# Optimization experiments

Measured on AMD Instinct MI355X. Metric: run time of the kernel, lower is better.

Reference implementation:

```python
import jax, jax.numpy as jnp
import numpy as np

N = 100000
E = 1600000
IN_FEATS = 512
N_CLASSES = 40
H1, D1 = 8, 8
H2, D2 = 1, N_CLASSES


def gat_conv(x, src, dst, W, al, ar, b, H, D):
    # x: [N, F] -> h: [N, H, D]
    n = x.shape[0]
    h = (x @ W).reshape(n, H, D)
    el = (h * al[None]).sum(-1)  # [N, H]
    er = (h * ar[None]).sum(-1)  # [N, H]
    e = jax.nn.leaky_relu(el[src] + er[dst], 0.2)  # [E, H]
    # segment softmax over destination neighborhoods
    emax = jax.ops.segment_max(e, dst, num_segments=n)  # [N, H]
    ee = jnp.exp(e - emax[dst])
    denom = jax.ops.segment_sum(ee, dst, num_segments=n)  # [N, H]
    a = ee / (denom[dst] + 1e-9)  # [E, H]
    m = h[src] * a[:, :, None]  # [E, H, D]
    out = jax.ops.segment_sum(m, dst, num_segments=n)  # [N, H, D]
    return out + b.reshape(1, H, D)


def setup_inputs() -> dict:
    key = jax.random.key(0)
    ks = jax.random.split(key, 12)
    g1 = 1.0 / np.sqrt(IN_FEATS)
    g2 = 1.0 / np.sqrt(H1 * D1)
    return {
        "x": jax.random.normal(ks[0], (N, IN_FEATS), jnp.float32),
        "src": jax.random.randint(ks[1], (E,), 0, N, jnp.int32),
        "dst": jax.random.randint(ks[2], (E,), 0, N, jnp.int32),
        "W1": jax.random.normal(ks[3], (IN_FEATS, H1 * D1), jnp.float32) * g1,
        "al1": jax.random.normal(ks[4], (H1, D1), jnp.float32) * 0.1,
        "ar1": jax.random.normal(ks[5], (H1, D1), jnp.float32) * 0.1,
        "b1": jnp.zeros((H1 * D1,), jnp.float32),
        "W2": jax.random.normal(ks[6], (H1 * D1, H2 * D2), jnp.float32) * g2,
        "al2": jax.random.normal(ks[7], (H2, D2), jnp.float32) * 0.1,
        "ar2": jax.random.normal(ks[8], (H2, D2), jnp.float32) * 0.1,
        "b2": jnp.zeros((H2 * D2,), jnp.float32),
    }


def reference(x, src, dst, W1, al1, ar1, b1, W2, al2, ar2, b2):
    h = gat_conv(x, src, dst, W1, al1, ar1, b1, H1, D1)  # [N, 8, 8]
    h = jax.nn.elu(h.reshape(N, H1 * D1))  # [N, 64]
    h = gat_conv(h, src, dst, W2, al2, ar2, b2, H2, D2).mean(axis=1)  # [N, n_classes]
    return jax.nn.log_softmax(h, axis=1)
```

## Files before the change

### kernel.cpp

```cpp
#include <hip/hip_runtime.h>
#include <hip/hip_bf16.h>
#include <math.h>

#define NCLS 40
#define PWG 256
#define BSH 9
#define NBMAX 512
#define SRCB 23
#define CSRCAP 14336

typedef __attribute__((ext_vector_type(8))) short bf16x8;
typedef __attribute__((ext_vector_type(4))) float f32x4;

__device__ inline float bf2f(ushort u) {
    unsigned v = ((unsigned)u) << 16;
    float f;
    __builtin_memcpy(&f, &v, 4);
    return f;
}
__device__ inline ushort f2bf(float f) {
    unsigned v;
    __builtin_memcpy(&v, &f, 4);
    unsigned r = (v + 0x7FFFu + ((v >> 16) & 1u)) >> 16;
    return (ushort)r;
}

__global__ __launch_bounds__(256) void conv_prep_kernel(
    const float* __restrict__ W1, ushort* __restrict__ W1t,
    const float* __restrict__ W2, const float* __restrict__ al2,
    const float* __restrict__ ar2, float* __restrict__ wal2,
    float* __restrict__ war2)
{
    if (blockIdx.x < 128) {
        int id = blockIdx.x * 256 + threadIdx.x;
        int k = id >> 6, c = id & 63;
        W1t[c * 512 + k] = f2bf(W1[k * 64 + c]);
    } else {
        int k = threadIdx.x;
        if (k < 64) {
            float a = 0.f, b = 0.f;
            for (int c = 0; c < NCLS; c++) {
                float w = W2[k * NCLS + c];
                a += w * al2[c];
                b += w * ar2[c];
            }
            wal2[k] = a;
            war2[k] = b;
        }
    }
}

__global__ __launch_bounds__(256) void gemm1_mfma_kernel(
    const float* __restrict__ x, const ushort* __restrict__ W1t,
    ushort* __restrict__ h1b, int Nn)
{
    __shared__ ushort As[64 * 40];
    __shared__ ushort Bs[64 * 40];
    const int t = threadIdx.x;
    const int lane = t & 63, w = t >> 6;
    const int tile = blockIdx.x * 64;

    f32x4 acc[4] = {};

    const int sr = t >> 2;
    const int sk = (t & 3) * 8;
    const int arow = tile + sr;
    const bool rowok = arow < Nn;
    const float* xrow = x + (size_t)arow * 512;
    const ushort* wrow = W1t + (size_t)sr * 512;

    const int r = lane & 15, g = lane >> 4;

    float4 f0, f1;
    bf16x8 bv;
    if (rowok) {
        f0 = *(const float4*)(xrow + sk);
        f1 = *(const float4*)(xrow + sk + 4);
    } else {
        f0 = make_float4(0.f, 0.f, 0.f, 0.f);
        f1 = f0;
    }
    bv = *(const bf16x8*)(wrow + sk);

    for (int k0 = 0; k0 < 512; k0 += 32) {
        bf16x8 av;
        av[0] = (short)f2bf(f0.x); av[1] = (short)f2bf(f0.y);
        av[2] = (short)f2bf(f0.z); av[3] = (short)f2bf(f0.w);
        av[4] = (short)f2bf(f1.x); av[5] = (short)f2bf(f1.y);
        av[6] = (short)f2bf(f1.z); av[7] = (short)f2bf(f1.w);
        *(bf16x8*)&As[sr * 40 + sk] = av;
        *(bf16x8*)&Bs[sr * 40 + sk] = bv;
        __syncthreads();

        int k1 = k0 + 32;
        if (k1 < 512) {
            if (rowok) {
                f0 = *(const float4*)(xrow + k1 + sk);
                f1 = *(const float4*)(xrow + k1 + sk + 4);
            }
            bv = *(const bf16x8*)(wrow + k1 + sk);
        }

        bf16x8 afrag = *(const bf16x8*)&As[(w * 16 + r) * 40 + g * 8];
#pragma unroll
        for (int cb = 0; cb < 4; cb++) {
            bf16x8 bfrag = *(const bf16x8*)&Bs[(cb * 16 + r) * 40 + g * 8];
            acc[cb] = __builtin_amdgcn_mfma_f32_16x16x32_bf16(afrag, bfrag, acc[cb], 0, 0, 0);
        }
        __syncthreads();
    }

#pragma unroll
    for (int cb = 0; cb < 4; cb++) {
#pragma unroll
        for (int v = 0; v < 4; v++) {
            int row = tile + w * 16 + g * 4 + v;
            if (row < Nn) h1b[(size_t)row * 64 + cb * 16 + r] = f2bf(acc[cb][v]);
        }
    }
}

__global__ __launch_bounds__(256) void elr1_kernel(
    const ushort* __restrict__ h1b, const float* __restrict__ al1,
    const float* __restrict__ ar1, float* __restrict__ el1,
    float* __restrict__ er1, int Nn)
{
    int id = blockIdx.x * 256 + threadIdx.x;
    if (id >= Nn * 8) return;
    int h = id & 7;
    const ushort* p = h1b + (size_t)id * 8;
    ushort4 u0 = *(const ushort4*)p;
    ushort4 u1 = *(const ushort4*)(p + 4);
    float v0 = bf2f(u0.x), v1 = bf2f(u0.y), v2 = bf2f(u0.z), v3 = bf2f(u0.w);
    float v4 = bf2f(u1.x), v5 = bf2f(u1.y), v6 = bf2f(u1.z), v7 = bf2f(u1.w);
    const float* a = al1 + h * 8;
    const float* b = ar1 + h * 8;
    el1[id] = v0 * a[0] + v1 * a[1] + v2 * a[2] + v3 * a[3] + v4 * a[4] + v5 * a[5] + v6 * a[6] + v7 * a[7];
    er1[id] = v0 * b[0] + v1 * b[1] + v2 * b[2] + v3 * b[3] + v4 * b[4] + v5 * b[5] + v6 * b[6] + v7 * b[7];
}

__global__ __launch_bounds__(256) void hist_kernel(const int* __restrict__ dst,
                                                   int* __restrict__ hist,
                                                   int Ee, int chunk, int NB)
{
    __shared__ int lh[NBMAX];
    const int wg = blockIdx.x, tid = threadIdx.x;
    for (int i = tid; i < NB; i += 256) lh[i] = 0;
    __syncthreads();
    const int beg = wg * chunk;
    const int endv = min(Ee, beg + chunk);
    for (int i = beg + tid; i < endv; i += 256) atomicAdd(&lh[dst[i] >> BSH], 1);
    __syncthreads();
    for (int b = tid; b < NB; b += 256) hist[b * PWG + wg] = lh[b];
}

__global__ __launch_bounds__(256) void scanA_kernel(int* __restrict__ hist,
                                                    int* __restrict__ bucketTot)
{
    __shared__ int s[256];
    const int b = blockIdx.x, tid = threadIdx.x;
    int v = hist[b * PWG + tid];
    s[tid] = v;
    __syncthreads();
#pragma unroll
    for (int o = 1; o < 256; o <<= 1) {
        int t = (tid >= o) ? s[tid - o] : 0;
        __syncthreads();
        s[tid] += t;
        __syncthreads();
    }
    hist[b * PWG + tid] = s[tid] - v;
    if (tid == 255) bucketTot[b] = s[255];
}

__global__ __launch_bounds__(256) void scanB_kernel(const int* __restrict__ bucketTot,
                                                    int* __restrict__ bucketBase,
                                                    int NB, int Ee)
{
    __shared__ int s[256];
    const int tid = threadIdx.x;
    int v = (tid < NB) ? bucketTot[tid] : 0;
    s[tid] = v;
    __syncthreads();
#pragma unroll
    for (int o = 1; o < 256; o <<= 1) {
        int t = (tid >= o) ? s[tid - o] : 0;
        __syncthreads();
        s[tid] += t;
        __syncthreads();
    }
    if (tid < NB) bucketBase[tid] = s[tid] - v;
    if (tid == 0) bucketBase[NB] = Ee;
}

__global__ __launch_bounds__(256) void partition_kernel(const int* __restrict__ src,
                                                        const int* __restrict__ dst,
                                                        const int* __restrict__ hist,
                                                        const int* __restrict__ bucketBase,
                                                        unsigned* __restrict__ ebuf,
                                                        int Ee, int chunk, int NB)
{
    __shared__ int cur[NBMAX];
    const int wg = blockIdx.x, tid = threadIdx.x;
    for (int b = tid; b < NB; b += 256) cur[b] = hist[b * PWG + wg] + bucketBase[b];
    __syncthreads();
    const int beg = wg * chunk;
    const int endv = min(Ee, beg + chunk);
    for (int i = beg + tid; i < endv; i += 256) {
        int d = dst[i];
        int p = atomicAdd(&cur[d >> BSH], 1);
        ebuf[p] = ((unsigned)(d & ((1 << BSH) - 1)) << SRCB) | (unsigned)src[i];
    }
}

__global__ __launch_bounds__(512) void bucket_csr_kernel(const unsigned* __restrict__ ebuf,
                                                         const int* __restrict__ bucketBase,
                                                         int* __restrict__ row_start,
                                                         int* __restrict__ perm_src,
                                                         int Nn, int Ee, int NB)
{
    __shared__ unsigned stage[CSRCAP];
    __shared__ int cnt[512];
    __shared__ int s[512];
    __shared__ int cur[512];
    const int b = blockIdx.x, tid = threadIdx.x;
    const int base = b << BSH;
    const int bb = bucketBase[b], be = bucketBase[b + 1];
    const int m = be - bb;

    cnt[tid] = 0;
    __syncthreads();
    for (int idx = tid; idx < m; idx += 512) {
        unsigned pk = ebuf[bb + idx];
        if (idx < CSRCAP) stage[idx] = pk;
        atomicAdd(&cnt[pk >> SRCB], 1);
    }
    __syncthreads();
    int v = cnt[tid];
    s[tid] = v;
    __syncthreads();
#pragma unroll
    for (int o = 1; o < 512; o <<= 1) {
        int t = (tid >= o) ? s[tid - o] : 0;
        __syncthreads();
        s[tid] += t;
        __syncthreads();
    }
    const int off = bb + s[tid] - v;
    const int node = base + tid;
    if (node < Nn) row_start[node] = off;
    cur[tid] = off;
    __syncthreads();
    for (int idx = tid; idx < m; idx += 512) {
        unsigned pk = (idx < CSRCAP) ? stage[idx] : ebuf[bb + idx];
        int p = atomicAdd(&cur[pk >> SRCB], 1);
        perm_src[p] = (int)(pk & ((1u << SRCB) - 1u));
    }
    if (b == NB - 1 && tid == 0) row_start[Nn] = Ee;
}

__global__ __launch_bounds__(256) void agg1_kernel(
    const ushort* __restrict__ h1b, const float* __restrict__ el1,
    const float* __restrict__ er1, const int* __restrict__ row_start,
    const int* __restrict__ perm_src, const float* __restrict__ b1,
    ushort* __restrict__ hmidb, int Nn)
{
    int wid = (blockIdx.x * blockDim.x + threadIdx.x) >> 6;
    int lane = threadIdx.x & 63;
    if (wid >= Nn) return;
    const int h = lane >> 3;
    const int beg = row_start[wid], end = row_start[wid + 1];
    const float er = er1[wid * 8 + h];

    float acc = 0.f, denom = 0.f;
    for (int i0 = beg; i0 < end; i0 += 64) {
        int cnt = min(end - i0, 64);
        int pv = (i0 + lane < end) ? perm_src[i0 + lane] : 0;
        int j = 0;
        for (; j + 8 <= cnt; j += 8) {
            int ss[8];
#pragma unroll
            for (int u = 0; u < 8; u++) ss[u] = __shfl(pv, j + u);
            float ev[8];
            ushort rv[8];
#pragma unroll
            for (int u = 0; u < 8; u++) ev[u] = el1[ss[u] * 8 + h];
#pragma unroll
            for (int u = 0; u < 8; u++) rv[u] = h1b[(size_t)ss[u] * 64 + lane];
#pragma unroll
            for (int u = 0; u < 8; u++) {
                float e = ev[u] + er;
                e = (e >= 0.f) ? e : 0.2f * e;
                float w = __expf(fminf(e, 80.f));
                denom += w;
                acc += bf2f(rv[u]) * w;
            }
        }
        for (; j + 4 <= cnt; j += 4) {
            int ss[4];
#pragma unroll
            for (int u = 0; u < 4; u++) ss[u] = __shfl(pv, j + u);
            float ev[4];
            ushort rv[4];
#pragma unroll
            for (int u = 0; u < 4; u++) ev[u] = el1[ss[u] * 8 + h];
#pragma unroll
            for (int u = 0; u < 4; u++) rv[u] = h1b[(size_t)ss[u] * 64 + lane];
#pragma unroll
            for (int u = 0; u < 4; u++) {
                float e = ev[u] + er;
                e = (e >= 0.f) ? e : 0.2f * e;
                float w = __expf(fminf(e, 80.f));
                denom += w;
                acc += bf2f(rv[u]) * w;
            }
        }
        for (; j < cnt; j++) {
            int sI = __shfl(pv, j);
            float e = el1[sI * 8 + h] + er;
            e = (e >= 0.f) ? e : 0.2f * e;
            float w = __expf(fminf(e, 80.f));
            denom += w;
            acc += bf2f(h1b[(size_t)sI * 64 + lane]) * w;
        }
    }
    float v = acc / (denom + 1e-9f) + b1[lane];
    v = (v > 0.f) ? v : expm1f(v);
    hmidb[(size_t)wid * 64 + lane] = f2bf(v);
}

__global__ __launch_bounds__(256) void gemm2_kernel(
    const ushort* __restrict__ hmidb, const float* __restrict__ W2,
    const float* __restrict__ wal2, const float* __restrict__ war2,
    ushort* __restrict__ h2b, float* __restrict__ el2, float* __restrict__ er2,
    int Nn)
{
    __shared__ float w2s[64 * NCLS];
    __shared__ float wals[64], wars[64];
    for (int i = threadIdx.x; i < 64 * NCLS; i += blockDim.x) w2s[i] = W2[i];
    if (threadIdx.x < 64) {
        wals[threadIdx.x] = wal2[threadIdx.x];
        wars[threadIdx.x] = war2[threadIdx.x];
    }
    __syncthreads();
    int n = blockIdx.x * blockDim.x + threadIdx.x;
    if (n >= Nn) return;

    float out[NCLS];
#pragma unroll
    for (int c = 0; c < NCLS; c++) out[c] = 0.f;
    float accel = 0.f, accer = 0.f;

#pragma unroll 4
    for (int k4 = 0; k4 < 16; k4++) {
        ushort4 u = *(const ushort4*)&hmidb[(size_t)n * 64 + k4 * 4];
        float h0 = bf2f(u.x), h1 = bf2f(u.y), h2 = bf2f(u.z), h3 = bf2f(u.w);
        accel += h0 * wals[k4 * 4] + h1 * wals[k4 * 4 + 1] + h2 * wals[k4 * 4 + 2] + h3 * wals[k4 * 4 + 3];
        accer += h0 * wars[k4 * 4] + h1 * wars[k4 * 4 + 1] + h2 * wars[k4 * 4 + 2] + h3 * wars[k4 * 4 + 3];
#pragma unroll
        for (int c = 0; c < NCLS; c++) {
            out[c] += h0 * w2s[(k4 * 4 + 0) * NCLS + c] + h1 * w2s[(k4 * 4 + 1) * NCLS + c] +
                      h2 * w2s[(k4 * 4 + 2) * NCLS + c] + h3 * w2s[(k4 * 4 + 3) * NCLS + c];
        }
    }
    el2[n] = accel;
    er2[n] = accer;
#pragma unroll
    for (int c = 0; c < NCLS; c++) h2b[(size_t)n * NCLS + c] = f2bf(out[c]);
}

__global__ __launch_bounds__(256) void agg2_kernel(
    const ushort* __restrict__ h2b, const float* __restrict__ el2,
    const float* __restrict__ er2, const int* __restrict__ row_start,
    const int* __restrict__ perm_src, const float* __restrict__ b2,
    float* __restrict__ out, int Nn)
{
    int wid = (blockIdx.x * blockDim.x + threadIdx.x) >> 6;
    int lane = threadIdx.x & 63;
    if (wid >= Nn) return;
    const int beg = row_start[wid], end = row_start[wid + 1];
    const float er = er2[wid];
    const bool act = lane < NCLS;
    const int cl = act ? lane : 0;

    float acc = 0.f, denom = 0.f;
    for (int i0 = beg; i0 < end; i0 += 64) {
        int cnt = min(end - i0, 64);
        int pv = (i0 + lane < end) ? perm_src[i0 + lane] : 0;
        int j = 0;
        for (; j + 8 <= cnt; j += 8) {
            int ss[8];
#pragma unroll
            for (int u = 0; u < 8; u++) ss[u] = __shfl(pv, j + u);
            float ev[8];
            ushort rv[8];
#pragma unroll
            for (int u = 0; u < 8; u++) ev[u] = el2[ss[u]];
#pragma unroll
            for (int u = 0; u < 8; u++) rv[u] = h2b[(size_t)ss[u] * NCLS + cl];
#pragma unroll
            for (int u = 0; u < 8; u++) {
                float e = ev[u] + er;
                e = (e >= 0.f) ? e : 0.2f * e;
                float w = __expf(fminf(e, 80.f));
                denom += w;
                acc += bf2f(rv[u]) * w;
            }
        }
        for (; j + 4 <= cnt; j += 4) {
            int ss[4];
#pragma unroll
            for (int u = 0; u < 4; u++) ss[u] = __shfl(pv, j + u);
            float ev[4];
            ushort rv[4];
#pragma unroll
            for (int u = 0; u < 4; u++) ev[u] = el2[ss[u]];
#pragma unroll
            for (int u = 0; u < 4; u++) rv[u] = h2b[(size_t)ss[u] * NCLS + cl];
#pragma unroll
            for (int u = 0; u < 4; u++) {
                float e = ev[u] + er;
                e = (e >= 0.f) ? e : 0.2f * e;
                float w = __expf(fminf(e, 80.f));
                denom += w;
                acc += bf2f(rv[u]) * w;
            }
        }
        for (; j < cnt; j++) {
            int sI = __shfl(pv, j);
            float e = el2[sI] + er;
            e = (e >= 0.f) ? e : 0.2f * e;
            float w = __expf(fminf(e, 80.f));
            denom += w;
            acc += bf2f(h2b[(size_t)sI * NCLS + cl]) * w;
        }
    }
    float v = act ? (acc / (denom + 1e-9f) + b2[lane]) : -1e30f;

    float mx = v;
#pragma unroll
    for (int o = 1; o < 64; o <<= 1) mx = fmaxf(mx, __shfl_xor(mx, o));
    float sx = act ? __expf(v - mx) : 0.f;
#pragma unroll
    for (int o = 1; o < 64; o <<= 1) sx += __shfl_xor(sx, o);
    if (act) out[(size_t)wid * NCLS + lane] = v - mx - __logf(sx);
}

extern "C" void kernel_launch(void* const* d_in, const int* in_sizes, int n_in,
                              void* d_out, int out_size, void* d_ws, size_t ws_size,
                              hipStream_t stream)
{
    const float* x   = (const float*)d_in[0];
    const int*   src = (const int*)d_in[1];
    const int*   dst = (const int*)d_in[2];
    const float* W1  = (const float*)d_in[3];
    const float* al1 = (const float*)d_in[4];
    const float* ar1 = (const float*)d_in[5];
    const float* b1  = (const float*)d_in[6];
    const float* W2  = (const float*)d_in[7];
    const float* al2 = (const float*)d_in[8];
    const float* ar2 = (const float*)d_in[9];
    const float* b2  = (const float*)d_in[10];
    float* out = (float*)d_out;

    const int Nn = in_sizes[0] / 512;
    const int Ee = in_sizes[1];
    const int NB = (Nn + (1 << BSH) - 1) >> BSH;
    const int chunk = (Ee + PWG - 1) / PWG;

    char* wsb = (char*)d_ws;
    size_t off = 0;
    auto alloc = [&](size_t bytes) -> void* {
        off = (off + 15) & ~(size_t)15;
        void* p = wsb + off;
        off += bytes;
        return p;
    };
    ushort* h1b   = (ushort*)alloc((size_t)Nn * 64 * 2);
    ushort* hmidb = (ushort*)alloc((size_t)Nn * 64 * 2);
    ushort* h2b   = (ushort*)alloc((size_t)Nn * NCLS * 2);
    ushort* W1t   = (ushort*)alloc(64 * 512 * 2);
    float* el1  = (float*)alloc((size_t)Nn * 8 * 4);
    float* er1  = (float*)alloc((size_t)Nn * 8 * 4);
    float* el2  = (float*)alloc((size_t)Nn * 4);
    float* er2  = (float*)alloc((size_t)Nn * 4);
    float* wal2 = (float*)alloc(64 * 4);
    float* war2 = (float*)alloc(64 * 4);
    int* row_start  = (int*)alloc((size_t)(Nn + 1) * 4);
    int* hist       = (int*)alloc((size_t)NB * PWG * 4);
    int* bucketTot  = (int*)alloc((size_t)NB * 4);
    int* bucketBase = (int*)alloc((size_t)(NB + 1) * 4);
    int* perm_src   = (int*)alloc((size_t)Ee * 4);
    unsigned* ebuf  = (unsigned*)alloc((size_t)Ee * 4);

    hist_kernel<<<PWG, 256, 0, stream>>>(dst, hist, Ee, chunk, NB);
    scanA_kernel<<<NB, 256, 0, stream>>>(hist, bucketTot);
    scanB_kernel<<<1, 256, 0, stream>>>(bucketTot, bucketBase, NB, Ee);
    partition_kernel<<<PWG, 256, 0, stream>>>(src, dst, hist, bucketBase, ebuf, Ee, chunk, NB);
    bucket_csr_kernel<<<NB, 512, 0, stream>>>(ebuf, bucketBase, row_start, perm_src, Nn, Ee, NB);

    conv_prep_kernel<<<129, 256, 0, stream>>>(W1, W1t, W2, al2, ar2, wal2, war2);
    gemm1_mfma_kernel<<<(Nn + 63) / 64, 256, 0, stream>>>(x, W1t, h1b, Nn);
    elr1_kernel<<<(Nn * 8 + 255) / 256, 256, 0, stream>>>(h1b, al1, ar1, el1, er1, Nn);
    agg1_kernel<<<(Nn + 3) / 4, 256, 0, stream>>>(h1b, el1, er1, row_start, perm_src, b1, hmidb, Nn);

    gemm2_kernel<<<(Nn + 255) / 256, 256, 0, stream>>>(hmidb, W2, wal2, war2, h2b, el2, er2, Nn);
    agg2_kernel<<<(Nn + 3) / 4, 256, 0, stream>>>(h2b, el2, er2, row_start, perm_src, b2, out, Nn);
}
```

Measured before the change: 265.4 us.

## Fuse el/er into GEMM1 epilogue, deepen K tile, unroll aggregation by 16, pad h2

Computes the layer-1 attention logits inside the MFMA GEMM epilogue using shuffle reductions, which removes the separate elr1 kernel and its reread of h1. The GEMM K-step is doubled to 64 so there are half as many barriers per tile. Both aggregation kernels now use a single 16-wide unrolled gather loop with masked tail weights in place of the 8/4/1 cascade, which gives more loads in flight but wastes lanes on short neighbourhoods. The h2 row stride is padded to 64 for aligned gathers, at the cost of extra memory.

```diff
diff --git a/kernel.cpp b/kernel.cpp
--- a/kernel.cpp
+++ b/kernel.cpp
@@ -3,6 +3,7 @@
 #include <math.h>
 
 #define NCLS 40
+#define H2S 64
 #define PWG 256
 #define BSH 9
 #define NBMAX 512
@@ -52,10 +53,12 @@
 
 __global__ __launch_bounds__(256) void gemm1_mfma_kernel(
     const float* __restrict__ x, const ushort* __restrict__ W1t,
-    ushort* __restrict__ h1b, int Nn)
-{
-    __shared__ ushort As[64 * 40];
-    __shared__ ushort Bs[64 * 40];
+    const float* __restrict__ al1, const float* __restrict__ ar1,
+    ushort* __restrict__ h1b, float* __restrict__ el1,
+    float* __restrict__ er1, int Nn)
+{
+    __shared__ ushort As[64 * 72];
+    __shared__ ushort Bs[64 * 72];
     const int t = threadIdx.x;
     const int lane = t & 63, w = t >> 6;
     const int tile = blockIdx.x * 64;
@@ -63,7 +66,7 @@
     f32x4 acc[4] = {};
 
     const int sr = t >> 2;
-    const int sk = (t & 3) * 8;
+    const int sk = (t & 3) * 16;
     const int arow = tile + sr;
     const bool rowok = arow < Nn;
     const float* xrow = x + (size_t)arow * 512;
@@ -71,72 +74,85 @@
 
     const int r = lane & 15, g = lane >> 4;
 
-    float4 f0, f1;
-    bf16x8 bv;
+    float4 f0 = make_float4(0.f, 0.f, 0.f, 0.f), f1 = f0, f2 = f0, f3 = f0;
+    bf16x8 bv0, bv1;
     if (rowok) {
         f0 = *(const float4*)(xrow + sk);
         f1 = *(const float4*)(xrow + sk + 4);
-    } else {
-        f0 = make_float4(0.f, 0.f, 0.f, 0.f);
-        f1 = f0;
-    }
-    bv = *(const bf16x8*)(wrow + sk);
-
-    for (int k0 = 0; k0 < 512; k0 += 32) {
-        bf16x8 av;
-        av[0] = (short)f2bf(f0.x); av[1] = (short)f2bf(f0.y);
-        av[2] = (short)f2bf(f0.z); av[3] = (short)f2bf(f0.w);
-        av[4] = (short)f2bf(f1.x); av[5] = (short)f2bf(f1.y);
-        av[6] = (short)f2bf(f1.z); av[7] = (short)f2bf(f1.w);
-        *(bf16x8*)&As[sr * 40 + sk] = av;
-        *(bf16x8*)&Bs[sr * 40 + sk] = bv;
-        __syncthreads();
-
-        int k1 = k0 + 32;
+        f2 = *(const float4*)(xrow + sk + 8);
+        f3 = *(const float4*)(xrow + sk + 12);
+    }
+    bv0 = *(const bf16x8*)(wrow + sk);
+    bv1 = *(const bf16x8*)(wrow + sk + 8);
+
+    for (int k0 = 0; k0 < 512; k0 += 64) {
+        bf16x8 av0, av1;
+        av0[0] = (short)f2bf(f0.x); av0[1] = (short)f2bf(f0.y);
+        av0[2] = (short)f2bf(f0.z); av0[3] = (short)f2bf(f0.w);
+        av0[4] = (short)f2bf(f1.x); av0[5] = (short)f2bf(f1.y);
+        av0[6] = (short)f2bf(f1.z); av0[7] = (short)f2bf(f1.w);
+        av1[0] = (short)f2bf(f2.x); av1[1] = (short)f2bf(f2.y);
+        av1[2] = (short)f2bf(f2.z); av1[3] = (short)f2bf(f2.w);
+        av1[4] = (short)f2bf(f3.x); av1[5] = (short)f2bf(f3.y);
+        av1[6] = (short)f2bf(f3.z); av1[7] = (short)f2bf(f3.w);
+        *(bf16x8*)&As[sr * 72 + sk] = av0;
+        *(bf16x8*)&As[sr * 72 + sk + 8] = av1;
+        *(bf16x8*)&Bs[sr * 72 + sk] = bv0;
+        *(bf16x8*)&Bs[sr * 72 + sk + 8] = bv1;
+        __syncthreads();
+
+        int k1 = k0 + 64;
         if (k1 < 512) {
             if (rowok) {
                 f0 = *(const float4*)(xrow + k1 + sk);
                 f1 = *(const float4*)(xrow + k1 + sk + 4);
+                f2 = *(const float4*)(xrow + k1 + sk + 8);
+                f3 = *(const float4*)(xrow + k1 + sk + 12);
             }
-            bv = *(const bf16x8*)(wrow + k1 + sk);
-        }
-
-        bf16x8 afrag = *(const bf16x8*)&As[(w * 16 + r) * 40 + g * 8];
+            bv0 = *(const bf16x8*)(wrow + k1 + sk);
+            bv1 = *(const bf16x8*)(wrow + k1 + sk + 8);
+        }
+
+        bf16x8 af0 = *(const bf16x8*)&As[(w * 16 + r) * 72 + g * 8];
+        bf16x8 af1 = *(const bf16x8*)&As[(w * 16 + r) * 72 + 32 + g * 8];
 #pragma unroll
         for (int cb = 0; cb < 4; cb++) {
-            bf16x8 bfrag = *(const bf16x8*)&Bs[(cb * 16 + r) * 40 + g * 8];
-            acc[cb] = __builtin_amdgcn_mfma_f32_16x16x32_bf16(afrag, bfrag, acc[cb], 0, 0, 0);
-        }
-        __syncthreads();
-    }
-
+            bf16x8 bf0 = *(const bf16x8*)&Bs[(cb * 16 + r) * 72 + g * 8];
+            acc[cb] = __builtin_amdgcn_mfma_f32_16x16x32_bf16(af0, bf0, acc[cb], 0, 0, 0);
+        }
+#pragma unroll
+        for (int cb = 0; cb < 4; cb++) {
+            bf16x8 bf1 = *(const bf16x8*)&Bs[(cb * 16 + r) * 72 + 32 + g * 8];
+            acc[cb] = __builtin_amdgcn_mfma_f32_16x16x32_bf16(af1, bf1, acc[cb], 0, 0, 0);
+        }
+        __syncthreads();
+    }
+
+    float alv[4], arv[4];
 #pragma unroll
     for (int cb = 0; cb < 4; cb++) {
-#pragma unroll
-        for (int v = 0; v < 4; v++) {
-            int row = tile + w * 16 + g * 4 + v;
-            if (row < Nn) h1b[(size_t)row * 64 + cb * 16 + r] = f2bf(acc[cb][v]);
-        }
-    }
-}
-
-__global__ __launch_bounds__(256) void elr1_kernel(
-    const ushort* __restrict__ h1b, const float* __restrict__ al1,
-    const float* __restrict__ ar1, float* __restrict__ el1,
-    float* __restrict__ er1, int Nn)
-{
-    int id = blockIdx.x * 256 + threadIdx.x;
-    if (id >= Nn * 8) return;
-    int h = id & 7;
-    const ushort* p = h1b + (size_t)id * 8;
-    ushort4 u0 = *(const ushort4*)p;
-    ushort4 u1 = *(const ushort4*)(p + 4);
-    float v0 = bf2f(u0.x), v1 = bf2f(u0.y), v2 = bf2f(u0.z), v3 = bf2f(u0.w);
-    float v4 = bf2f(u1.x), v5 = bf2f(u1.y), v6 = bf2f(u1.z), v7 = bf2f(u1.w);
-    const float* a = al1 + h * 8;
-    const float* b = ar1 + h * 8;
-    el1[id] = v0 * a[0] + v1 * a[1] + v2 * a[2] + v3 * a[3] + v4 * a[4] + v5 * a[5] + v6 * a[6] + v7 * a[7];
-    er1[id] = v0 * b[0] + v1 * b[1] + v2 * b[2] + v3 * b[3] + v4 * b[4] + v5 * b[5] + v6 * b[6] + v7 * b[7];
+        alv[cb] = al1[cb * 16 + r];
+        arv[cb] = ar1[cb * 16 + r];
+    }
+#pragma unroll
+    for (int v = 0; v < 4; v++) {
+        int row = tile + w * 16 + g * 4 + v;
+        bool ok = row < Nn;
+#pragma unroll
+        for (int cb = 0; cb < 4; cb++) {
+            if (ok) h1b[(size_t)row * 64 + cb * 16 + r] = f2bf(acc[cb][v]);
+            float pel = acc[cb][v] * alv[cb];
+            float per = acc[cb][v] * arv[cb];
+            pel += __shfl_xor(pel, 1); per += __shfl_xor(per, 1);
+            pel += __shfl_xor(pel, 2); per += __shfl_xor(per, 2);
+            pel += __shfl_xor(pel, 4); per += __shfl_xor(per, 4);
+            if (ok && (r & 7) == 0) {
+                int head = cb * 2 + (r >> 3);
+                el1[row * 8 + head] = pel;
+                er1[row * 8 + head] = per;
+            }
+        }
+    }
 }
 
 __global__ __launch_bounds__(256) void hist_kernel(const int* __restrict__ dst,
@@ -274,54 +290,26 @@
 
     float acc = 0.f, denom = 0.f;
     for (int i0 = beg; i0 < end; i0 += 64) {
-        int cnt = min(end - i0, 64);
+        const int cnt = min(end - i0, 64);
         int pv = (i0 + lane < end) ? perm_src[i0 + lane] : 0;
-        int j = 0;
-        for (; j + 8 <= cnt; j += 8) {
-            int ss[8];
-#pragma unroll
-            for (int u = 0; u < 8; u++) ss[u] = __shfl(pv, j + u);
-            float ev[8];
-            ushort rv[8];
-#pragma unroll
-            for (int u = 0; u < 8; u++) ev[u] = el1[ss[u] * 8 + h];
-#pragma unroll
-            for (int u = 0; u < 8; u++) rv[u] = h1b[(size_t)ss[u] * 64 + lane];
-#pragma unroll
-            for (int u = 0; u < 8; u++) {
+        for (int j = 0; j < cnt; j += 16) {
+            int ss[16];
+            float ev[16];
+            ushort rv[16];
+#pragma unroll
+            for (int u = 0; u < 16; u++) ss[u] = __shfl(pv, min(j + u, cnt - 1));
+#pragma unroll
+            for (int u = 0; u < 16; u++) ev[u] = el1[ss[u] * 8 + h];
+#pragma unroll
+            for (int u = 0; u < 16; u++) rv[u] = h1b[(size_t)ss[u] * 64 + lane];
+#pragma unroll
+            for (int u = 0; u < 16; u++) {
                 float e = ev[u] + er;
                 e = (e >= 0.f) ? e : 0.2f * e;
-                float w = __expf(fminf(e, 80.f));
-                denom += w;
-                acc += bf2f(rv[u]) * w;
+                float wgt = (j + u < cnt) ? __expf(fminf(e, 80.f)) : 0.f;
+                denom += wgt;
+                acc += bf2f(rv[u]) * wgt;
             }
-        }
-        for (; j + 4 <= cnt; j += 4) {
-            int ss[4];
-#pragma unroll
-            for (int u = 0; u < 4; u++) ss[u] = __shfl(pv, j + u);
-            float ev[4];
-            ushort rv[4];
-#pragma unroll
-            for (int u = 0; u < 4; u++) ev[u] = el1[ss[u] * 8 + h];
-#pragma unroll
-            for (int u = 0; u < 4; u++) rv[u] = h1b[(size_t)ss[u] * 64 + lane];
-#pragma unroll
-            for (int u = 0; u < 4; u++) {
-                float e = ev[u] + er;
-                e = (e >= 0.f) ? e : 0.2f * e;
-                float w = __expf(fminf(e, 80.f));
-                denom += w;
-                acc += bf2f(rv[u]) * w;
-            }
-        }
-        for (; j < cnt; j++) {
-            int sI = __shfl(pv, j);
-            float e = el1[sI * 8 + h] + er;
-            e = (e >= 0.f) ? e : 0.2f * e;
-            float w = __expf(fminf(e, 80.f));
-            denom += w;
-            acc += bf2f(h1b[(size_t)sI * 64 + lane]) * w;
         }
     }
     float v = acc / (denom + 1e-9f) + b1[lane];
@@ -366,7 +354,7 @@
     el2[n] = accel;
     er2[n] = accer;
 #pragma unroll
-    for (int c = 0; c < NCLS; c++) h2b[(size_t)n * NCLS + c] = f2bf(out[c]);
+    for (int c = 0; c < NCLS; c++) h2b[(size_t)n * H2S + c] = f2bf(out[c]);
 }
 
 __global__ __launch_bounds__(256) void agg2_kernel(
@@ -385,54 +373,26 @@
 
     float acc = 0.f, denom = 0.f;
     for (int i0 = beg; i0 < end; i0 += 64) {
-        int cnt = min(end - i0, 64);
+        const int cnt = min(end - i0, 64);
         int pv = (i0 + lane < end) ? perm_src[i0 + lane] : 0;
-        int j = 0;
-        for (; j + 8 <= cnt; j += 8) {
-            int ss[8];
-#pragma unroll
-            for (int u = 0; u < 8; u++) ss[u] = __shfl(pv, j + u);
-            float ev[8];
-            ushort rv[8];
-#pragma unroll
-            for (int u = 0; u < 8; u++) ev[u] = el2[ss[u]];
-#pragma unroll
-            for (int u = 0; u < 8; u++) rv[u] = h2b[(size_t)ss[u] * NCLS + cl];
-#pragma unroll
-            for (int u = 0; u < 8; u++) {
+        for (int j = 0; j < cnt; j += 16) {
+            int ss[16];
+            float ev[16];
+            ushort rv[16];
+#pragma unroll
+            for (int u = 0; u < 16; u++) ss[u] = __shfl(pv, min(j + u, cnt - 1));
+#pragma unroll
+            for (int u = 0; u < 16; u++) ev[u] = el2[ss[u]];
+#pragma unroll
+            for (int u = 0; u < 16; u++) rv[u] = h2b[(size_t)ss[u] * H2S + cl];
+#pragma unroll
+            for (int u = 0; u < 16; u++) {
                 float e = ev[u] + er;
                 e = (e >= 0.f) ? e : 0.2f * e;
-                float w = __expf(fminf(e, 80.f));
-                denom += w;
-                acc += bf2f(rv[u]) * w;
+                float wgt = (j + u < cnt) ? __expf(fminf(e, 80.f)) : 0.f;
+                denom += wgt;
+                acc += bf2f(rv[u]) * wgt;
             }
-        }
-        for (; j + 4 <= cnt; j += 4) {
-            int ss[4];
-#pragma unroll
-            for (int u = 0; u < 4; u++) ss[u] = __shfl(pv, j + u);
-            float ev[4];
-            ushort rv[4];
-#pragma unroll
-            for (int u = 0; u < 4; u++) ev[u] = el2[ss[u]];
-#pragma unroll
-            for (int u = 0; u < 4; u++) rv[u] = h2b[(size_t)ss[u] * NCLS + cl];
-#pragma unroll
-            for (int u = 0; u < 4; u++) {
-                float e = ev[u] + er;
-                e = (e >= 0.f) ? e : 0.2f * e;
-                float w = __expf(fminf(e, 80.f));
-                denom += w;
-                acc += bf2f(rv[u]) * w;
-            }
-        }
-        for (; j < cnt; j++) {
-            int sI = __shfl(pv, j);
-            float e = el2[sI] + er;
-            e = (e >= 0.f) ? e : 0.2f * e;
-            float w = __expf(fminf(e, 80.f));
-            denom += w;
-            acc += bf2f(h2b[(size_t)sI * NCLS + cl]) * w;
         }
     }
     float v = act ? (acc / (denom + 1e-9f) + b2[lane]) : -1e30f;
@@ -478,7 +438,7 @@
     };
     ushort* h1b   = (ushort*)alloc((size_t)Nn * 64 * 2);
     ushort* hmidb = (ushort*)alloc((size_t)Nn * 64 * 2);
-    ushort* h2b   = (ushort*)alloc((size_t)Nn * NCLS * 2);
+    ushort* h2b   = (ushort*)alloc((size_t)Nn * H2S * 2);
     ushort* W1t   = (ushort*)alloc(64 * 512 * 2);
     float* el1  = (float*)alloc((size_t)Nn * 8 * 4);
     float* er1  = (float*)alloc((size_t)Nn * 8 * 4);
@@ -500,8 +460,7 @@
     bucket_csr_kernel<<<NB, 512, 0, stream>>>(ebuf, bucketBase, row_start, perm_src, Nn, Ee, NB);
 
     conv_prep_kernel<<<129, 256, 0, stream>>>(W1, W1t, W2, al2, ar2, wal2, war2);
-    gemm1_mfma_kernel<<<(Nn + 63) / 64, 256, 0, stream>>>(x, W1t, h1b, Nn);
-    elr1_kernel<<<(Nn * 8 + 255) / 256, 256, 0, stream>>>(h1b, al1, ar1, el1, er1, Nn);
+    gemm1_mfma_kernel<<<(Nn + 63) / 64, 256, 0, stream>>>(x, W1t, al1, ar1, h1b, el1, er1, Nn);
     agg1_kernel<<<(Nn + 3) / 4, 256, 0, stream>>>(h1b, el1, er1, row_start, perm_src, b1, hmidb, Nn);
 
     gemm2_kernel<<<(Nn + 255) / 256, 256, 0, stream>>>(hmidb, W2, wal2, war2, h2b, el2, er2, Nn);
```

After: 338.2 us. 27.4% more time.
